# Performance work log

Hardware: AMD Instinct MI355X
Metric: run time of the kernel (lower is better)

The kernel has to match this reference:

```python
import jax, jax.numpy as jnp
import numpy as np

S, N, D, H = 4096, 16384, 768, 768  # n_slots, n_inputs, feature_size(=dim), mlp hidden
ITERS = 3
SCALE = D ** -0.5
LN_EPS = 1e-5  # torch LayerNorm default


def _ln(x, g, b):
    m = jnp.mean(x, axis=-1, keepdims=True)
    v = jnp.var(x, axis=-1, keepdims=True)
    return (x - m) * jax.lax.rsqrt(v + LN_EPS) * g + b


def setup_inputs() -> dict:
    key = jax.random.key(0)
    ks = jax.random.split(key, 16)
    w = lambda k, shp: jax.random.normal(k, shp, dtype=jnp.float32) * 0.02
    return {
        "cand_feat": jax.random.normal(ks[0], (S, D), dtype=jnp.float32),
        "pano_feat": jax.random.normal(ks[1], (N, D), dtype=jnp.float32),
        "Wq": w(ks[2], (D, D)), "bq": jnp.zeros((D,), jnp.float32),
        "Wk": w(ks[3], (D, D)), "bk": jnp.zeros((D,), jnp.float32),
        "Wv": w(ks[4], (D, D)), "bv": jnp.zeros((D,), jnp.float32),
        "W_ih": w(ks[5], (3 * D, D)), "b_ih": jnp.zeros((3 * D,), jnp.float32),
        "W_hh": w(ks[6], (3 * D, D)), "b_hh": jnp.zeros((3 * D,), jnp.float32),
        "W1": w(ks[7], (H, D)), "b1": jnp.zeros((H,), jnp.float32),
        "W2": w(ks[8], (D, H)), "b2": jnp.zeros((D,), jnp.float32),
        "g_in": jnp.ones((D,), jnp.float32), "be_in": jnp.zeros((D,), jnp.float32),
        "g_sl": jnp.ones((D,), jnp.float32), "be_sl": jnp.zeros((D,), jnp.float32),
        "g_ff": jnp.ones((D,), jnp.float32), "be_ff": jnp.zeros((D,), jnp.float32),
    }


def reference(cand_feat, pano_feat, Wq, bq, Wk, bk, Wv, bv,
              W_ih, b_ih, W_hh, b_hh, W1, b1, W2, b2,
              g_in, be_in, g_sl, be_sl, g_ff, be_ff):
    # dropout layers act as identity at inference
    slots = cand_feat                       # [S, D]
    pano = _ln(pano_feat, g_in, be_in)      # [N, D]
    k = pano @ Wk.T + bk                    # [N, D]
    v = pano @ Wv.T + bv                    # [N, D]
    for _ in range(ITERS):
        slots_prev = slots
        q = _ln(slots, g_sl, be_sl) @ Wq.T + bq          # [S, D]
        dots = jnp.einsum('id,jd->ij', q, k) * SCALE     # [S, N]
        attn = jax.nn.softmax(dots, axis=1)
        updates = jnp.einsum('jd,ij->id', v, attn)       # [S, D]
        # torch.nn.GRUCell(updates, slots_prev)
        gx = updates @ W_ih.T + b_ih                     # [S, 3D]
        gh = slots_prev @ W_hh.T + b_hh                  # [S, 3D]
        xr, xz, xn = jnp.split(gx, 3, axis=-1)
        hr, hz, hn = jnp.split(gh, 3, axis=-1)
        r = jax.nn.sigmoid(xr + hr)
        z = jax.nn.sigmoid(xz + hz)
        n = jnp.tanh(xn + r * hn)
        h = (1.0 - z) * n + z * slots_prev               # [S, D]
        ff = _ln(h, g_ff, be_ff)
        slots = h + (jax.nn.relu(ff @ W1.T + b1) @ W2.T + b2)
    return slots
```

## Files before the change

kernel.cpp:

```cpp
#include <hip/hip_runtime.h>
#include <cstdint>
#include <cstddef>

typedef __bf16 bf16;
typedef __bf16 bf16x8 __attribute__((ext_vector_type(8)));
typedef __bf16 bf16x4 __attribute__((ext_vector_type(4)));
typedef float f32x4 __attribute__((ext_vector_type(4)));
typedef long long i64;

#define S_DIM 4096
#define N_DIM 16384
#define D_DIM 768
#define NCHUNK 8192
#define NZ 8
#define KSLICE (NCHUNK / NZ)

static constexpr float SCALE = 0.03608439182435161f;

__device__ inline void gl_lds16(const void* g, void* l) {
  __builtin_amdgcn_global_load_lds((const __attribute__((address_space(1))) void*)g,
                                   (__attribute__((address_space(3))) void*)l, 16, 0, 0);
}

__device__ inline unsigned char to_fp8(float x) {
  int p = __builtin_amdgcn_cvt_pk_fp8_f32(x, x, 0, false);
  return (unsigned char)(p & 0xff);
}

struct GemmArgs {
  const bf16* A; const bf16* B;
  const float* bias;
  float* outF; bf16* outB; unsigned char* outP8;
  const float* res;
  float* lsum;
  int M, N, K, lda, ldb;
  float scale;
};

template<int EPIL>
__device__ __forceinline__ void gemm_core(const GemmArgs& g, const int bm, const int bn,
                                          bf16* sA, bf16* sB) {
  const int tid  = threadIdx.x;
  const int wave = tid >> 6;
  const int lane = tid & 63;
  const int quad = lane >> 4;
  const int l15  = lane & 15;
  const int wm = (wave >> 1) * 64;
  const int wn = (wave & 1) * 64;

  f32x4 acc[4][4];
#pragma unroll
  for (int t = 0; t < 4; ++t)
#pragma unroll
    for (int u = 0; u < 4; ++u) acc[t][u] = (f32x4){0.f, 0.f, 0.f, 0.f};

  const int s0 = wave * 64 + lane;
  const int s1 = 256 + s0;
  const int r0 = s0 >> 2, c0 = s0 & 3, x0 = (r0 & 3) ^ ((r0 >> 2) & 3);
  const int r1 = s1 >> 2, c1 = s1 & 3, x1 = (r1 & 3) ^ ((r1 >> 2) & 3);
  const size_t lda = (size_t)g.lda, ldb = (size_t)g.ldb;
  const bf16* gA0 = g.A + (size_t)(bm + r0) * lda + (c0 ^ x0) * 8;
  const bf16* gA1 = g.A + (size_t)(bm + r1) * lda + (c1 ^ x1) * 8;
  const bf16* gB0 = g.B + (size_t)(bn + r0) * ldb + (c0 ^ x0) * 8;
  const bf16* gB1 = g.B + (size_t)(bn + r1) * ldb + (c1 ^ x1) * 8;
  bf16* lA0 = sA + s0 * 8;  bf16* lA1 = sA + s1 * 8;
  bf16* lB0 = sB + s0 * 8;  bf16* lB1 = sB + s1 * 8;

  const int xr = (l15 & 3) ^ ((l15 >> 2) & 3);
  const int qx = (quad ^ xr) * 8;

  for (int k0 = 0; k0 < g.K; k0 += 32) {
    __syncthreads();
    gl_lds16(gA0 + k0, lA0);
    gl_lds16(gA1 + k0, lA1);
    gl_lds16(gB0 + k0, lB0);
    gl_lds16(gB1 + k0, lB1);
    __syncthreads();
    bf16x8 af[4], bv[4];
#pragma unroll
    for (int t = 0; t < 4; ++t)
      af[t] = *(const bf16x8*)(sA + (wm + t * 16 + l15) * 32 + qx);
#pragma unroll
    for (int u = 0; u < 4; ++u)
      bv[u] = *(const bf16x8*)(sB + (wn + u * 16 + l15) * 32 + qx);
#pragma unroll
    for (int t = 0; t < 4; ++t)
#pragma unroll
      for (int u = 0; u < 4; ++u)
        acc[t][u] = __builtin_amdgcn_mfma_f32_16x16x32_bf16(af[t], bv[u], acc[t][u], 0, 0, 0);
  }

  const int ldc = g.N;
#pragma unroll
  for (int t = 0; t < 4; ++t) {
    const int rbase = bm + wm + t * 16 + quad * 4;
    if (EPIL == 10) {
      float rsum[4] = {0.f, 0.f, 0.f, 0.f};
#pragma unroll
      for (int u = 0; u < 4; ++u) {
        const int col = bn + wn + u * 16 + l15;
#pragma unroll
        for (int r = 0; r < 4; ++r) {
          float e = __expf(acc[t][u][r] * g.scale);
          g.outP8[(size_t)(rbase + r) * ldc + col] = to_fp8(e);
          rsum[r] += e;
        }
      }
#pragma unroll
      for (int m = 1; m < 16; m <<= 1)
#pragma unroll
        for (int r = 0; r < 4; ++r) rsum[r] += __shfl_xor(rsum[r], m, 64);
      if (l15 == 0)
#pragma unroll
        for (int r = 0; r < 4; ++r) atomicAdd(&g.lsum[rbase + r], rsum[r]);
    } else {
#pragma unroll
      for (int u = 0; u < 4; ++u) {
        const int col = bn + wn + u * 16 + l15;
        const float cbias = (EPIL == 0 || EPIL == 4 || EPIL == 5) ? g.bias[col] : 0.f;
#pragma unroll
        for (int r = 0; r < 4; ++r) {
          const size_t idx = (size_t)(rbase + r) * ldc + col;
          const float v = acc[t][u][r];
          if (EPIL == 0) g.outB[idx] = (bf16)(v + cbias);
          else if (EPIL == 4) { float x = v + cbias; g.outB[idx] = (bf16)(x > 0.f ? x : 0.f); }
          else if (EPIL == 5) g.outF[idx] = v + cbias + g.res[idx];
          else if (EPIL == 9) g.outP8[idx] = to_fp8(v + g.bias[rbase + r]);
        }
      }
    }
  }
}

#define GEMM_SHARED __shared__ __align__(16) bf16 sA[128 * 32]; __shared__ __align__(16) bf16 sB[128 * 32]

__global__ __launch_bounds__(256) void k_dots(GemmArgs g) {
  GEMM_SHARED; gemm_core<10>(g, blockIdx.y * 128, blockIdx.x * 128, sA, sB);
}
__global__ __launch_bounds__(256) void k_qgemm(GemmArgs g) {
  GEMM_SHARED; gemm_core<0>(g, blockIdx.y * 128, blockIdx.x * 128, sA, sB);
}
__global__ __launch_bounds__(256) void k_kgemm(GemmArgs g) {
  GEMM_SHARED; gemm_core<0>(g, blockIdx.y * 128, blockIdx.x * 128, sA, sB);
}
__global__ __launch_bounds__(256) void k_vtgemm(GemmArgs g) {
  GEMM_SHARED; gemm_core<9>(g, blockIdx.y * 128, blockIdx.x * 128, sA, sB);
}
__global__ __launch_bounds__(256) void k_relu(GemmArgs g) {
  GEMM_SHARED; gemm_core<4>(g, blockIdx.y * 128, blockIdx.x * 128, sA, sB);
}
__global__ __launch_bounds__(256) void k_resid(GemmArgs g) {
  GEMM_SHARED; gemm_core<5>(g, blockIdx.y * 128, blockIdx.x * 128, sA, sB);
}
__global__ __launch_bounds__(256) void k_dual(GemmArgs a, GemmArgs b, int split) {
  GEMM_SHARED;
  if ((int)blockIdx.x < split) gemm_core<0>(a, blockIdx.y * 128, blockIdx.x * 128, sA, sB);
  else                         gemm_core<0>(b, blockIdx.y * 128, (blockIdx.x - split) * 128, sA, sB);
}

struct F8Args {
  const unsigned char* A; const unsigned char* B;
  bf16* out;
  int lda, ldb;
};

template<int INIT>
__global__ __launch_bounds__(512) void k_upd(F8Args u) {
  __shared__ __align__(16) unsigned char sA[128 * 32];
  __shared__ __align__(16) unsigned char sB[256 * 32];
  const int tid  = threadIdx.x;
  const int wave = tid >> 6;
  const int lane = tid & 63;
  const int quad = lane >> 4;
  const int l15  = lane & 15;
  const int bm = blockIdx.y * 128;
  const int bn = blockIdx.x * 256;
  const int z  = blockIdx.z;
  const int wm = (wave >> 2) * 64;
  const int wn = (wave & 3) * 64;

  const unsigned char* A = u.A + (size_t)z * KSLICE;
  const unsigned char* B = u.B + (size_t)z * KSLICE;
  bf16* out = u.out + (size_t)z * S_DIM * D_DIM;

  f32x4 acc[4][4];
#pragma unroll
  for (int t = 0; t < 4; ++t)
#pragma unroll
    for (int u2 = 0; u2 < 4; ++u2) acc[t][u2] = (f32x4){0.f, 0.f, 0.f, 0.f};

  const size_t lda = (size_t)u.lda, ldb = (size_t)u.ldb;
  const int rb = tid >> 1, hb = tid & 1;
  const unsigned char* gB = B + (size_t)(bn + rb) * ldb + ((hb ^ ((rb >> 2) & 1)) * 16);
  unsigned char* lB = sB + tid * 16;
  const int ta = tid & 255;
  const int ra = ta >> 1, ha = ta & 1;
  const unsigned char* gA = A + (size_t)(bm + ra) * lda + ((ha ^ ((ra >> 2) & 1)) * 16);
  unsigned char* lA = sA + ta * 16;
  const bool doA = (tid < 256);

  const int xh = (l15 >> 2) & 1;
  const int qoff = (((quad >> 1) ^ xh) * 16) + (quad & 1) * 8;

  for (int k0 = 0; k0 < KSLICE; k0 += 32) {
    __syncthreads();
    if (doA) gl_lds16(gA + k0, lA);
    gl_lds16(gB + k0, lB);
    __syncthreads();
    i64 af[4], bv[4];
#pragma unroll
    for (int t = 0; t < 4; ++t)
      af[t] = *(const i64*)(sA + (wm + t * 16 + l15) * 32 + qoff);
#pragma unroll
    for (int u2 = 0; u2 < 4; ++u2)
      bv[u2] = *(const i64*)(sB + (wn + u2 * 16 + l15) * 32 + qoff);
#pragma unroll
    for (int t = 0; t < 4; ++t)
#pragma unroll
      for (int u2 = 0; u2 < 4; ++u2)
        acc[t][u2] = __builtin_amdgcn_mfma_f32_16x16x32_fp8_fp8(af[t], bv[u2], acc[t][u2], 0, 0, 0);
  }

#pragma unroll
  for (int t = 0; t < 4; ++t) {
    const int rbase = bm + wm + t * 16 + quad * 4;
#pragma unroll
    for (int u2 = 0; u2 < 4; ++u2) {
      const int col = bn + wn + u2 * 16 + l15;
#pragma unroll
      for (int r = 0; r < 4; ++r) {
        const size_t idx = (size_t)(rbase + r) * D_DIM + col;
        if (INIT) out[idx] = (bf16)acc[t][u2][r];
        else      out[idx] = (bf16)((float)out[idx] + acc[t][u2][r]);
      }
    }
  }
}

__global__ void reduce_div_k(const bf16* __restrict__ bufs, const float* __restrict__ lsum,
                             bf16* __restrict__ out) {
  const int idx = blockIdx.x * 256 + threadIdx.x;
  const int row = idx / 192;
  const float inv = 1.0f / lsum[row];
  float s0 = 0.f, s1 = 0.f, s2 = 0.f, s3 = 0.f;
#pragma unroll
  for (int z = 0; z < NZ; ++z) {
    bf16x4 v = ((const bf16x4*)(bufs + (size_t)z * S_DIM * D_DIM))[idx];
    s0 += (float)v[0]; s1 += (float)v[1]; s2 += (float)v[2]; s3 += (float)v[3];
  }
  bf16x4 y;
  y[0] = (bf16)(s0 * inv); y[1] = (bf16)(s1 * inv);
  y[2] = (bf16)(s2 * inv); y[3] = (bf16)(s3 * inv);
  ((bf16x4*)out)[idx] = y;
}

__global__ void ln_stats_k(const float* __restrict__ X, float2* __restrict__ st) {
  const int row  = blockIdx.x * 4 + (threadIdx.x >> 6);
  const int lane = threadIdx.x & 63;
  const float4* xr = (const float4*)(X + (size_t)row * 768);
  float s = 0.f, ss = 0.f;
#pragma unroll
  for (int i = 0; i < 3; ++i) {
    float4 v = xr[lane + 64 * i];
    s  += v.x + v.y + v.z + v.w;
    ss += v.x * v.x + v.y * v.y + v.z * v.z + v.w * v.w;
  }
#pragma unroll
  for (int m = 1; m < 64; m <<= 1) { s += __shfl_xor(s, m, 64); ss += __shfl_xor(ss, m, 64); }
  if (lane == 0) {
    float mean = s * (1.f / 768.f);
    float var  = ss * (1.f / 768.f) - mean * mean;
    st[row] = make_float2(mean, rsqrtf(var + 1e-5f));
  }
}

__global__ void ln_apply_k(const float* __restrict__ X, const float2* __restrict__ st,
                           const float* __restrict__ gam, const float* __restrict__ bet,
                           bf16* __restrict__ Y) {
  const int idx = blockIdx.x * 256 + threadIdx.x;
  const int row = idx / 192, c4 = idx % 192;
  const float2 s = st[row];
  float4 x  = ((const float4*)(X + (size_t)row * 768))[c4];
  float4 g4 = ((const float4*)gam)[c4];
  float4 b4 = ((const float4*)bet)[c4];
  bf16x4 y;
  y[0] = (bf16)((x.x - s.x) * s.y * g4.x + b4.x);
  y[1] = (bf16)((x.y - s.x) * s.y * g4.y + b4.y);
  y[2] = (bf16)((x.z - s.x) * s.y * g4.z + b4.z);
  y[3] = (bf16)((x.w - s.x) * s.y * g4.w + b4.w);
  ((bf16x4*)(Y + (size_t)row * 768))[c4] = y;
}

__global__ void cvt_k(const float* __restrict__ X, bf16* __restrict__ Y) {
  const int i = blockIdx.x * 256 + threadIdx.x;
  float4 v = ((const float4*)X)[i];
  bf16x4 y;
  y[0] = (bf16)v.x; y[1] = (bf16)v.y; y[2] = (bf16)v.z; y[3] = (bf16)v.w;
  ((bf16x4*)Y)[i] = y;
}

__device__ inline float gru1(float xr, float xz, float xn, float hr, float hz, float hn, float sp) {
  float r = 1.f / (1.f + __expf(-(xr + hr)));
  float z = 1.f / (1.f + __expf(-(xz + hz)));
  float n = tanhf(xn + r * hn);
  return (1.f - z) * n + z * sp;
}

__global__ void gru_gate_k(const bf16* __restrict__ gx, const bf16* __restrict__ gh,
                           const float* __restrict__ slots, float* __restrict__ h) {
  const int idx = blockIdx.x * 256 + threadIdx.x;
  const int row = idx / 192, c4 = idx % 192;
  const bf16x4* gxr = (const bf16x4*)(gx + (size_t)row * 2304);
  const bf16x4* ghr = (const bf16x4*)(gh + (size_t)row * 2304);
  bf16x4 xr = gxr[c4], xz = gxr[192 + c4], xn = gxr[384 + c4];
  bf16x4 hr = ghr[c4], hz = ghr[192 + c4], hn = ghr[384 + c4];
  float4 sp = ((const float4*)(slots + (size_t)row * 768))[c4];
  float4 o;
  o.x = gru1((float)xr[0], (float)xz[0], (float)xn[0], (float)hr[0], (float)hz[0], (float)hn[0], sp.x);
  o.y = gru1((float)xr[1], (float)xz[1], (float)xn[1], (float)hr[1], (float)hz[1], (float)hn[1], sp.y);
  o.z = gru1((float)xr[2], (float)xz[2], (float)xn[2], (float)hr[2], (float)hz[2], (float)hn[2], sp.z);
  o.w = gru1((float)xr[3], (float)xz[3], (float)xn[3], (float)hr[3], (float)hz[3], (float)hn[3], sp.w);
  ((float4*)(h + (size_t)row * 768))[c4] = o;
}

extern "C" void kernel_launch(void* const* d_in, const int* in_sizes, int n_in,
                              void* d_out, int out_size, void* d_ws, size_t ws_size,
                              hipStream_t stream) {
  (void)in_sizes; (void)n_in; (void)out_size; (void)ws_size;
  const float* cand  = (const float*)d_in[0];
  const float* pano  = (const float*)d_in[1];
  const float* Wq  = (const float*)d_in[2];  const float* bq  = (const float*)d_in[3];
  const float* Wk  = (const float*)d_in[4];  const float* bk  = (const float*)d_in[5];
  const float* Wv  = (const float*)d_in[6];  const float* bv  = (const float*)d_in[7];
  const float* Wih = (const float*)d_in[8];  const float* bih = (const float*)d_in[9];
  const float* Whh = (const float*)d_in[10]; const float* bhh = (const float*)d_in[11];
  const float* W1  = (const float*)d_in[12]; const float* b1  = (const float*)d_in[13];
  const float* W2  = (const float*)d_in[14]; const float* b2  = (const float*)d_in[15];
  const float* g_in = (const float*)d_in[16]; const float* be_in = (const float*)d_in[17];
  const float* g_sl = (const float*)d_in[18]; const float* be_sl = (const float*)d_in[19];
  const float* g_ff = (const float*)d_in[20]; const float* be_ff = (const float*)d_in[21];

  const size_t WU = (size_t)D_DIM * D_DIM;

  char* base = (char*)d_ws;
  size_t off = 0;
  auto alloc = [&](size_t bytes) -> void* {
    void* r = base + off;
    off = (off + bytes + 255) & ~(size_t)255;
    return r;
  };

  bf16* wq_bf  = (bf16*)alloc(WU * 2);
  bf16* wk_bf  = (bf16*)alloc(WU * 2);
  bf16* wv_bf  = (bf16*)alloc(WU * 2);
  bf16* wih_bf = (bf16*)alloc(3 * WU * 2);
  bf16* whh_bf = (bf16*)alloc(3 * WU * 2);
  bf16* w1_bf  = (bf16*)alloc(WU * 2);
  bf16* w2_bf  = (bf16*)alloc(WU * 2);
  bf16* k_bf   = (bf16*)alloc((size_t)N_DIM * D_DIM * 2);
  unsigned char* vt_f8 = (unsigned char*)alloc((size_t)N_DIM * D_DIM);
  float* slots = (float*)alloc((size_t)S_DIM * D_DIM * 4);
  bf16* slots_bf = (bf16*)alloc((size_t)S_DIM * D_DIM * 2);
  float2* statsP = (float2*)alloc((size_t)N_DIM * 8);
  float2* statsS = (float2*)alloc((size_t)S_DIM * 8);
  bf16* slotsln = (bf16*)alloc((size_t)S_DIM * D_DIM * 2);
  bf16* q_bf    = (bf16*)alloc((size_t)S_DIM * D_DIM * 2);
  bf16* upd_bf  = (bf16*)alloc((size_t)S_DIM * D_DIM * 2);
  bf16* hln_bf  = (bf16*)alloc((size_t)S_DIM * D_DIM * 2);
  bf16* m1_bf   = (bf16*)alloc((size_t)S_DIM * D_DIM * 2);
  float* lsum   = (float*)alloc((size_t)S_DIM * 4);
  const size_t PCH = (size_t)S_DIM * NCHUNK;
  const size_t PBF = (size_t)NZ * S_DIM * D_DIM * 2;
  char* arena = (char*)alloc(PCH + PBF);
  bf16* panoln = (bf16*)arena;
  unsigned char* Pchunk = (unsigned char*)arena;
  bf16* pbufs = (bf16*)(arena + PCH);
  bf16* gx = (bf16*)arena;
  bf16* gh = (bf16*)(arena + (size_t)S_DIM * 3 * D_DIM * 2);
  float* hbuf = (float*)(arena + 2 * (size_t)S_DIM * 3 * D_DIM * 2);

  cvt_k<<<dim3(WU / 1024), 256, 0, stream>>>(Wq, wq_bf);
  cvt_k<<<dim3(WU / 1024), 256, 0, stream>>>(Wk, wk_bf);
  cvt_k<<<dim3(WU / 1024), 256, 0, stream>>>(Wv, wv_bf);
  cvt_k<<<dim3(3 * WU / 1024), 256, 0, stream>>>(Wih, wih_bf);
  cvt_k<<<dim3(3 * WU / 1024), 256, 0, stream>>>(Whh, whh_bf);
  cvt_k<<<dim3(WU / 1024), 256, 0, stream>>>(W1, w1_bf);
  cvt_k<<<dim3(WU / 1024), 256, 0, stream>>>(W2, w2_bf);

  ln_stats_k<<<dim3(N_DIM / 4), 256, 0, stream>>>(pano, statsP);
  ln_apply_k<<<dim3(N_DIM * 192 / 256), 256, 0, stream>>>(pano, statsP, g_in, be_in, panoln);
  {
    GemmArgs ak{};
    ak.A = panoln; ak.B = wk_bf; ak.bias = bk; ak.outB = k_bf;
    ak.M = N_DIM; ak.N = D_DIM; ak.K = D_DIM; ak.lda = D_DIM; ak.ldb = D_DIM;
    k_kgemm<<<dim3(6, 128), 256, 0, stream>>>(ak);
    GemmArgs av{};
    av.A = wv_bf; av.B = panoln; av.bias = bv; av.outP8 = vt_f8;
    av.M = D_DIM; av.N = N_DIM; av.K = D_DIM; av.lda = D_DIM; av.ldb = D_DIM;
    k_vtgemm<<<dim3(128, 6), 256, 0, stream>>>(av);
  }

  hipMemcpyAsync(slots, cand, (size_t)S_DIM * D_DIM * 4, hipMemcpyDeviceToDevice, stream);
  cvt_k<<<dim3(S_DIM * D_DIM / 1024), 256, 0, stream>>>(cand, slots_bf);

  for (int iter = 0; iter < 3; ++iter) {
    ln_stats_k<<<dim3(S_DIM / 4), 256, 0, stream>>>(slots, statsS);
    ln_apply_k<<<dim3(S_DIM * 192 / 256), 256, 0, stream>>>(slots, statsS, g_sl, be_sl, slotsln);
    GemmArgs aq{};
    aq.A = slotsln; aq.B = wq_bf; aq.bias = bq; aq.outB = q_bf;
    aq.M = S_DIM; aq.N = D_DIM; aq.K = D_DIM; aq.lda = D_DIM; aq.ldb = D_DIM;
    k_qgemm<<<dim3(6, 32), 256, 0, stream>>>(aq);

    hipMemsetAsync(lsum, 0, (size_t)S_DIM * 4, stream);
    for (int c = 0; c < N_DIM / NCHUNK; ++c) {
      GemmArgs ad{};
      ad.A = q_bf; ad.B = k_bf + (size_t)c * NCHUNK * D_DIM;
      ad.outP8 = Pchunk; ad.lsum = lsum; ad.scale = SCALE;
      ad.M = S_DIM; ad.N = NCHUNK; ad.K = D_DIM; ad.lda = D_DIM; ad.ldb = D_DIM;
      k_dots<<<dim3(NCHUNK / 128, S_DIM / 128), 256, 0, stream>>>(ad);

      F8Args au{};
      au.A = Pchunk; au.B = vt_f8 + (size_t)c * NCHUNK;
      au.out = pbufs; au.lda = NCHUNK; au.ldb = N_DIM;
      if (c == 0) k_upd<1><<<dim3(3, 32, NZ), 512, 0, stream>>>(au);
      else        k_upd<0><<<dim3(3, 32, NZ), 512, 0, stream>>>(au);
    }
    reduce_div_k<<<dim3(S_DIM * 192 / 256), 256, 0, stream>>>(pbufs, lsum, upd_bf);

    {
      GemmArgs agx{};
      agx.A = upd_bf; agx.B = wih_bf; agx.bias = bih; agx.outB = gx;
      agx.M = S_DIM; agx.N = 3 * D_DIM; agx.K = D_DIM; agx.lda = D_DIM; agx.ldb = D_DIM;
      GemmArgs agh{};
      agh.A = slots_bf; agh.B = whh_bf; agh.bias = bhh; agh.outB = gh;
      agh.M = S_DIM; agh.N = 3 * D_DIM; agh.K = D_DIM; agh.lda = D_DIM; agh.ldb = D_DIM;
      k_dual<<<dim3(36, 32), 256, 0, stream>>>(agx, agh, 18);
    }
    gru_gate_k<<<dim3(S_DIM * 192 / 256), 256, 0, stream>>>(gx, gh, slots, hbuf);

    ln_stats_k<<<dim3(S_DIM / 4), 256, 0, stream>>>(hbuf, statsS);
    ln_apply_k<<<dim3(S_DIM * 192 / 256), 256, 0, stream>>>(hbuf, statsS, g_ff, be_ff, hln_bf);
    GemmArgs am1{};
    am1.A = hln_bf; am1.B = w1_bf; am1.bias = b1; am1.outB = m1_bf;
    am1.M = S_DIM; am1.N = D_DIM; am1.K = D_DIM; am1.lda = D_DIM; am1.ldb = D_DIM;
    k_relu<<<dim3(6, 32), 256, 0, stream>>>(am1);
    GemmArgs am2{};
    am2.A = m1_bf; am2.B = w2_bf; am2.bias = b2; am2.res = hbuf;
    am2.outF = (iter == 2) ? (float*)d_out : slots;
    am2.M = S_DIM; am2.N = D_DIM; am2.K = D_DIM; am2.lda = D_DIM; am2.ldb = D_DIM;
    k_resid<<<dim3(6, 32), 256, 0, stream>>>(am2);

    if (iter < 2)
      cvt_k<<<dim3(S_DIM * D_DIM / 1024), 256, 0, stream>>>(slots, slots_bf);
  }
}
```

Measured before the change: 1.763 ms.

## Process full N in one pass with a 128x256 dots tile and no chunking

Removes the two-chunk loop over N, so the whole fp8 probability matrix is materialized at once and the P·V update kernel runs a single pass with larger K slices. This drops the read-modify-write accumulation into the partial buffers that the second chunk needed. The dots GEMM becomes a dedicated 512-thread kernel with a 128x256 tile for more reuse of the loaded tiles. hln and m1 now alias existing buffers to save memory. The cost is a larger arena (the full S×N fp8 matrix) and more memory traffic per launch.

```diff
diff --git a/kernel.cpp b/kernel.cpp
--- a/kernel.cpp
+++ b/kernel.cpp
@@ -11,9 +11,8 @@
 #define S_DIM 4096
 #define N_DIM 16384
 #define D_DIM 768
-#define NCHUNK 8192
 #define NZ 8
-#define KSLICE (NCHUNK / NZ)
+#define KSLICE (N_DIM / NZ)
 
 static constexpr float SCALE = 0.03608439182435161f;
 
@@ -94,39 +93,18 @@
 #pragma unroll
   for (int t = 0; t < 4; ++t) {
     const int rbase = bm + wm + t * 16 + quad * 4;
-    if (EPIL == 10) {
-      float rsum[4] = {0.f, 0.f, 0.f, 0.f};
-#pragma unroll
-      for (int u = 0; u < 4; ++u) {
-        const int col = bn + wn + u * 16 + l15;
-#pragma unroll
-        for (int r = 0; r < 4; ++r) {
-          float e = __expf(acc[t][u][r] * g.scale);
-          g.outP8[(size_t)(rbase + r) * ldc + col] = to_fp8(e);
-          rsum[r] += e;
-        }
-      }
-#pragma unroll
-      for (int m = 1; m < 16; m <<= 1)
-#pragma unroll
-        for (int r = 0; r < 4; ++r) rsum[r] += __shfl_xor(rsum[r], m, 64);
-      if (l15 == 0)
-#pragma unroll
-        for (int r = 0; r < 4; ++r) atomicAdd(&g.lsum[rbase + r], rsum[r]);
-    } else {
-#pragma unroll
-      for (int u = 0; u < 4; ++u) {
-        const int col = bn + wn + u * 16 + l15;
-        const float cbias = (EPIL == 0 || EPIL == 4 || EPIL == 5) ? g.bias[col] : 0.f;
-#pragma unroll
-        for (int r = 0; r < 4; ++r) {
-          const size_t idx = (size_t)(rbase + r) * ldc + col;
-          const float v = acc[t][u][r];
-          if (EPIL == 0) g.outB[idx] = (bf16)(v + cbias);
-          else if (EPIL == 4) { float x = v + cbias; g.outB[idx] = (bf16)(x > 0.f ? x : 0.f); }
-          else if (EPIL == 5) g.outF[idx] = v + cbias + g.res[idx];
-          else if (EPIL == 9) g.outP8[idx] = to_fp8(v + g.bias[rbase + r]);
-        }
+#pragma unroll
+    for (int u = 0; u < 4; ++u) {
+      const int col = bn + wn + u * 16 + l15;
+      const float cbias = (EPIL == 0 || EPIL == 4 || EPIL == 5) ? g.bias[col] : 0.f;
+#pragma unroll
+      for (int r = 0; r < 4; ++r) {
+        const size_t idx = (size_t)(rbase + r) * ldc + col;
+        const float v = acc[t][u][r];
+        if (EPIL == 0) g.outB[idx] = (bf16)(v + cbias);
+        else if (EPIL == 4) { float x = v + cbias; g.outB[idx] = (bf16)(x > 0.f ? x : 0.f); }
+        else if (EPIL == 5) g.outF[idx] = v + cbias + g.res[idx];
+        else if (EPIL == 9) g.outP8[idx] = to_fp8(v + g.bias[rbase + r]);
       }
     }
   }
@@ -134,9 +112,6 @@
 
 #define GEMM_SHARED __shared__ __align__(16) bf16 sA[128 * 32]; __shared__ __align__(16) bf16 sB[128 * 32]
 
-__global__ __launch_bounds__(256) void k_dots(GemmArgs g) {
-  GEMM_SHARED; gemm_core<10>(g, blockIdx.y * 128, blockIdx.x * 128, sA, sB);
-}
 __global__ __launch_bounds__(256) void k_qgemm(GemmArgs g) {
   GEMM_SHARED; gemm_core<0>(g, blockIdx.y * 128, blockIdx.x * 128, sA, sB);
 }
@@ -156,6 +131,84 @@
   GEMM_SHARED;
   if ((int)blockIdx.x < split) gemm_core<0>(a, blockIdx.y * 128, blockIdx.x * 128, sA, sB);
   else                         gemm_core<0>(b, blockIdx.y * 128, (blockIdx.x - split) * 128, sA, sB);
+}
+
+__global__ __launch_bounds__(512) void k_dots(GemmArgs g) {
+  __shared__ __align__(16) bf16 sA[128 * 32];
+  __shared__ __align__(16) bf16 sB[256 * 32];
+  const int tid  = threadIdx.x;
+  const int wave = tid >> 6;
+  const int lane = tid & 63;
+  const int quad = lane >> 4;
+  const int l15  = lane & 15;
+  const int bm = blockIdx.y * 128;
+  const int bn = blockIdx.x * 256;
+  const int wm = (wave >> 2) * 64;
+  const int wn = (wave & 3) * 64;
+
+  f32x4 acc[4][4];
+#pragma unroll
+  for (int t = 0; t < 4; ++t)
+#pragma unroll
+    for (int u = 0; u < 4; ++u) acc[t][u] = (f32x4){0.f, 0.f, 0.f, 0.f};
+
+  const size_t lda = (size_t)g.lda, ldb = (size_t)g.ldb;
+  const int sa = tid,        raA = sa >> 2, caA = sa & 3, xaA = (raA & 3) ^ ((raA >> 2) & 3);
+  const int sb0 = tid,       rb0 = sb0 >> 2, cb0 = sb0 & 3, xb0 = (rb0 & 3) ^ ((rb0 >> 2) & 3);
+  const int sb1 = tid + 512, rb1 = sb1 >> 2, cb1 = sb1 & 3, xb1 = (rb1 & 3) ^ ((rb1 >> 2) & 3);
+  const bf16* gA  = g.A + (size_t)(bm + raA) * lda + (caA ^ xaA) * 8;
+  const bf16* gB0 = g.B + (size_t)(bn + rb0) * ldb + (cb0 ^ xb0) * 8;
+  const bf16* gB1 = g.B + (size_t)(bn + rb1) * ldb + (cb1 ^ xb1) * 8;
+  bf16* lA  = sA + sa * 8;
+  bf16* lB0 = sB + sb0 * 8;
+  bf16* lB1 = sB + sb1 * 8;
+
+  const int xr = (l15 & 3) ^ ((l15 >> 2) & 3);
+  const int qx = (quad ^ xr) * 8;
+
+  for (int k0 = 0; k0 < D_DIM; k0 += 32) {
+    __syncthreads();
+    gl_lds16(gA + k0, lA);
+    gl_lds16(gB0 + k0, lB0);
+    gl_lds16(gB1 + k0, lB1);
+    __syncthreads();
+    bf16x8 af[4], bv[4];
+#pragma unroll
+    for (int t = 0; t < 4; ++t)
+      af[t] = *(const bf16x8*)(sA + (wm + t * 16 + l15) * 32 + qx);
+#pragma unroll
+    for (int u = 0; u < 4; ++u)
+      bv[u] = *(const bf16x8*)(sB + (wn + u * 16 + l15) * 32 + qx);
+#pragma unroll
+    for (int t = 0; t < 4; ++t)
+#pragma unroll
+      for (int u = 0; u < 4; ++u)
+        acc[t][u] = __builtin_amdgcn_mfma_f32_16x16x32_bf16(af[t], bv[u], acc[t][u], 0, 0, 0);
+  }
+
+  const int ldc = g.N;
+#pragma unroll
+  for (int t = 0; t < 4; ++t) {
+    const int rbase = bm + wm + t * 16 + quad * 4;
+    float rsum[4] = {0.f, 0.f, 0.f, 0.f};
+#pragma unroll
+    for (int u = 0; u < 4; ++u) {
+      const int col = bn + wn + u * 16 + l15;
+#pragma unroll
+      for (int r = 0; r < 4; ++r) {
+        float e = __expf(acc[t][u][r] * g.scale);
+        g.outP8[(size_t)(rbase + r) * ldc + col] = to_fp8(e);
+        rsum[r] += e;
+      }
+    }
+#pragma unroll
+    for (int m = 1; m < 16; m <<= 1)
+#pragma unroll
+      for (int r = 0; r < 4; ++r) rsum[r] += __shfl_xor(rsum[r], m, 64);
+    if (l15 == 0)
+#pragma unroll
+      for (int r = 0; r < 4; ++r) atomicAdd(&g.lsum[rbase + r], rsum[r]);
+  }
 }
 
 struct F8Args {
@@ -164,7 +217,6 @@
   int lda, ldb;
 };
 
-template<int INIT>
 __global__ __launch_bounds__(512) void k_upd(F8Args u) {
   __shared__ __align__(16) unsigned char sA[128 * 32];
   __shared__ __align__(16) unsigned char sB[256 * 32];
@@ -228,11 +280,8 @@
     for (int u2 = 0; u2 < 4; ++u2) {
       const int col = bn + wn + u2 * 16 + l15;
 #pragma unroll
-      for (int r = 0; r < 4; ++r) {
-        const size_t idx = (size_t)(rbase + r) * D_DIM + col;
-        if (INIT) out[idx] = (bf16)acc[t][u2][r];
-        else      out[idx] = (bf16)((float)out[idx] + acc[t][u2][r]);
-      }
+      for (int r = 0; r < 4; ++r)
+        out[(size_t)(rbase + r) * D_DIM + col] = (bf16)acc[t][u2][r];
     }
   }
 }
@@ -366,14 +415,14 @@
   bf16* slotsln = (bf16*)alloc((size_t)S_DIM * D_DIM * 2);
   bf16* q_bf    = (bf16*)alloc((size_t)S_DIM * D_DIM * 2);
   bf16* upd_bf  = (bf16*)alloc((size_t)S_DIM * D_DIM * 2);
-  bf16* hln_bf  = (bf16*)alloc((size_t)S_DIM * D_DIM * 2);
-  bf16* m1_bf   = (bf16*)alloc((size_t)S_DIM * D_DIM * 2);
   float* lsum   = (float*)alloc((size_t)S_DIM * 4);
-  const size_t PCH = (size_t)S_DIM * NCHUNK;
+  bf16* hln_bf = slotsln;
+  bf16* m1_bf  = q_bf;
+  const size_t PCH = (size_t)S_DIM * N_DIM;
   const size_t PBF = (size_t)NZ * S_DIM * D_DIM * 2;
   char* arena = (char*)alloc(PCH + PBF);
   bf16* panoln = (bf16*)arena;
-  unsigned char* Pchunk = (unsigned char*)arena;
+  unsigned char* Pfull = (unsigned char*)arena;
   bf16* pbufs = (bf16*)(arena + PCH);
   bf16* gx = (bf16*)arena;
   bf16* gh = (bf16*)(arena + (size_t)S_DIM * 3 * D_DIM * 2);
@@ -412,18 +461,17 @@
     k_qgemm<<<dim3(6, 32), 256, 0, stream>>>(aq);
 
     hipMemsetAsync(lsum, 0, (size_t)S_DIM * 4, stream);
-    for (int c = 0; c < N_DIM / NCHUNK; ++c) {
+    {
       GemmArgs ad{};
-      ad.A = q_bf; ad.B = k_bf + (size_t)c * NCHUNK * D_DIM;
-      ad.outP8 = Pchunk; ad.lsum = lsum; ad.scale = SCALE;
-      ad.M = S_DIM; ad.N = NCHUNK; ad.K = D_DIM; ad.lda = D_DIM; ad.ldb = D_DIM;
-      k_dots<<<dim3(NCHUNK / 128, S_DIM / 128), 256, 0, stream>>>(ad);
+      ad.A = q_bf; ad.B = k_bf;
+      ad.outP8 = Pfull; ad.lsum = lsum; ad.scale = SCALE;
+      ad.M = S_DIM; ad.N = N_DIM; ad.K = D_DIM; ad.lda = D_DIM; ad.ldb = D_DIM;
+      k_dots<<<dim3(N_DIM / 256, S_DIM / 128), 512, 0, stream>>>(ad);
 
       F8Args au{};
-      au.A = Pchunk; au.B = vt_f8 + (size_t)c * NCHUNK;
-      au.out = pbufs; au.lda = NCHUNK; au.ldb = N_DIM;
-      if (c == 0) k_upd<1><<<dim3(3, 32, NZ), 512, 0, stream>>>(au);
-      else        k_upd<0><<<dim3(3, 32, NZ), 512, 0, stream>>>(au);
+      au.A = Pfull; au.B = vt_f8;
+      au.out = pbufs; au.lda = N_DIM; au.ldb = N_DIM;
+      k_upd<<<dim3(3, 32, NZ), 512, 0, stream>>>(au);
     }
     reduce_div_k<<<dim3(S_DIM * 192 / 256), 256, 0, stream>>>(pbufs, lsum, upd_bf);
 
```

New measurement: 1.935 ms. +9.8%, slower.
